# Kernel tuning notes

Measured on AMD Instinct MI355X. Metric: run time of the kernel, lower is better.

The kernel has to match this reference:

```python
import jax, jax.numpy as jnp
import numpy as np

HIDDEN = 512

def setup_inputs() -> dict:
    key = jax.random.key(0)
    kx, kq, kk, kv = jax.random.split(key, 4)
    B, S, H = 4, 4096, HIDDEN
    scale = 1.0 / np.sqrt(H)
    x = jax.random.normal(kx, (B, S, H), dtype=jnp.float32)
    # nn.Linear weights are [out, in]; y = x @ W.T
    Wq = jax.random.normal(kq, (H, H), dtype=jnp.float32) * scale
    Wk = jax.random.normal(kk, (H, H), dtype=jnp.float32) * scale
    Wv = jax.random.normal(kv, (H, H), dtype=jnp.float32) * scale
    return {"x": x, "Wq": Wq, "Wk": Wk, "Wv": Wv}

def reference(x, Wq, Wk, Wv):
    H = x.shape[-1]
    q = jnp.einsum('bsh,oh->bso', x, Wq)
    k = jnp.einsum('bsh,oh->bso', x, Wk)
    v = jnp.einsum('bsh,oh->bso', x, Wv)
    scores = jnp.einsum('bqh,bkh->bqk', q, k) / jnp.sqrt(jnp.asarray(H, x.dtype))
    att = jax.nn.softmax(scores, axis=-1)  # max-subtracted softmax, same math as manual version
    return jnp.einsum('bqk,bkh->bqh', att, v)
```

## Files before the change

### kernel.cpp

```cpp
#include <hip/hip_runtime.h>
#include <stdint.h>

typedef unsigned short u16;
typedef __bf16  bf16x8   __attribute__((ext_vector_type(8)));
typedef float   floatx4  __attribute__((ext_vector_type(4)));
typedef unsigned short ushortx4 __attribute__((ext_vector_type(4)));

__device__ __forceinline__ u16 f2bf(float f) {
  unsigned u = __builtin_bit_cast(unsigned, f);
  u += 0x7FFFu + ((u >> 16) & 1u);
  return (u16)(u >> 16);
}

#define GLD_LDS16(g, l)                                                        \
  __builtin_amdgcn_global_load_lds(                                            \
      (const __attribute__((address_space(1))) void*)(g),                      \
      (__attribute__((address_space(3))) void*)(l), 16, 0, 0)

#define VMW(N) asm volatile("s_waitcnt vmcnt(" #N ")" ::: "memory")

__global__ __launch_bounds__(256) void cvt_w(
    const float* __restrict__ Wq, const float* __restrict__ Wk,
    const float* __restrict__ Wv, u16* __restrict__ dst)
{
  const int z = blockIdx.y;
  const float* src = (z == 0) ? Wq : (z == 1) ? Wk : Wv;
  u16* d = dst + (size_t)z * 262144;
  const int idx = (blockIdx.x * 256 + threadIdx.x) * 8;
  const float4 lo = *(const float4*)&src[idx];
  const float4 hi = *(const float4*)&src[idx + 4];
  union { u16 h[8]; uint4 v; } pk;
  pk.h[0] = f2bf(lo.x); pk.h[1] = f2bf(lo.y); pk.h[2] = f2bf(lo.z); pk.h[3] = f2bf(lo.w);
  pk.h[4] = f2bf(hi.x); pk.h[5] = f2bf(hi.y); pk.h[6] = f2bf(hi.z); pk.h[7] = f2bf(hi.w);
  *(uint4*)&d[idx] = pk.v;
}

__global__ __launch_bounds__(256) void cvt_x(
    const float* __restrict__ X, u16* __restrict__ dst)
{
  const int idx = (blockIdx.x * 256 + threadIdx.x) * 8;
  const float4 lo = *(const float4*)&X[idx];
  const float4 hi = *(const float4*)&X[idx + 4];
  union { u16 h[8]; uint4 v; } pk;
  pk.h[0] = f2bf(lo.x); pk.h[1] = f2bf(lo.y); pk.h[2] = f2bf(lo.z); pk.h[3] = f2bf(lo.w);
  pk.h[4] = f2bf(hi.x); pk.h[5] = f2bf(hi.y); pk.h[6] = f2bf(hi.z); pk.h[7] = f2bf(hi.w);
  *(uint4*)&dst[idx] = pk.v;
}

__global__ __launch_bounds__(512, 2) void qkv8(
    const u16* __restrict__ X16, const u16* __restrict__ Wb,
    u16* __restrict__ qo, u16* __restrict__ ko, u16* __restrict__ vto)
{
  __shared__ u16 lds[65536];

  const int tid = threadIdx.x;
  const int w  = tid >> 6, l = tid & 63;
  const int lr = l & 15, lq = l >> 4;
  const int wA = (w & 1) * 16;
  const int wB = (w >> 1) * 16;

  const int bx = blockIdx.x;
  const int li = (bx & 7) * 48 + (bx >> 3);
  const int z  = li >> 7, u = li & 127;

  const u16* Ag; const u16* Bg; u16* dst; float sc; size_t ostr; int mb, nb;
  if (z < 2) {
    Ag = Wb + (size_t)z * 262144; Bg = X16;
    dst = z ? ko : qo; sc = z ? 1.0f : 0.06375871732f; ostr = 512;
    mb = (u & 1) * 256;  nb = (u >> 1) * 256;
  } else {
    Ag = X16; Bg = Wb + (size_t)2 * 262144;
    dst = vto; sc = 1.0f; ostr = 16384;
    mb = (u >> 1) * 256; nb = (u & 1) * 256;
  }

  floatx4 acc[8][4];
  const floatx4 fz = {0.f, 0.f, 0.f, 0.f};
#pragma unroll
  for (int i = 0; i < 8; ++i)
#pragma unroll
    for (int j = 0; j < 4; ++j) acc[i][j] = fz;

  auto stage = [&](int s) {
    const int ts = s >> 2, kind = s & 3;
    const int mat = kind & 1, h = kind >> 1;
    const u16* src = mat ? Bg : Ag;
    const int rbase = mat ? nb : mb;
    u16* dstl = &lds[(ts & 1) * 32768 + mat * 16384];
#pragma unroll
    for (int i = 0; i < 2; ++i) {
      const int c = i * 512 + tid;
      const int r = h * 128 + (c >> 3), k16 = c & 7;
      const int k16s = k16 ^ (r & 7);
      GLD_LDS16(src + (size_t)(rbase + r) * 512 + ts * 64 + k16s * 8,
                &dstl[r * 64 + k16 * 8]);
    }
  };

#pragma unroll
  for (int s = 0; s < 6; ++s) stage(s);
  VMW(4);
  __builtin_amdgcn_s_barrier();
  __builtin_amdgcn_sched_barrier(0);

  bf16x8 af[4][2];
  bf16x8 bf0[2][2], bf1[2][2];

#pragma unroll
  for (int t = 0; t < 8; ++t) {
#pragma unroll
    for (int qd = 0; qd < 4; ++qd) {
      const int fmh = qd >> 1;
      const int fnh = fmh ^ (qd & 1);
      const u16* AB = &lds[(t & 1) * 32768];
      const u16* BB = AB + 16384;

      if (qd == 0 || qd == 2) {
#pragma unroll
        for (int im = 0; im < 4; ++im) {
          const int rA = (fmh * 4 + im) * 32 + wA + lr;
#pragma unroll
          for (int ks = 0; ks < 2; ++ks) {
            const int k16p = (ks * 4 + lq) ^ (rA & 7);
            af[im][ks] = *(const bf16x8*)&AB[rA * 64 + k16p * 8];
          }
        }
      }
      if (qd == 0) {
#pragma unroll
        for (int jn = 0; jn < 2; ++jn) {
          const int rB = jn * 64 + wB + lr;
#pragma unroll
          for (int ks = 0; ks < 2; ++ks) {
            const int k16p = (ks * 4 + lq) ^ (rB & 7);
            bf0[jn][ks] = *(const bf16x8*)&BB[rB * 64 + k16p * 8];
          }
        }
      }
      if (qd == 1) {
#pragma unroll
        for (int jn = 0; jn < 2; ++jn) {
          const int rB = (2 + jn) * 64 + wB + lr;
#pragma unroll
          for (int ks = 0; ks < 2; ++ks) {
            const int k16p = (ks * 4 + lq) ^ (rB & 7);
            bf1[jn][ks] = *(const bf16x8*)&BB[rB * 64 + k16p * 8];
          }
        }
      }

      const int s = t * 4 + qd + 6;
      if (s < 32) stage(s);

      __builtin_amdgcn_sched_barrier(0);
      __builtin_amdgcn_s_barrier();
      asm volatile("s_waitcnt lgkmcnt(0)" ::: "memory");
      __builtin_amdgcn_sched_barrier(0);

      __builtin_amdgcn_s_setprio(1);
      if (fnh) {
#pragma unroll
        for (int im = 0; im < 4; ++im)
#pragma unroll
          for (int jn = 0; jn < 2; ++jn)
#pragma unroll
            for (int ks = 0; ks < 2; ++ks)
              acc[fmh * 4 + im][2 + jn] =
                  __builtin_amdgcn_mfma_f32_16x16x32_bf16(
                      af[im][ks], bf1[jn][ks], acc[fmh * 4 + im][2 + jn], 0, 0, 0);
      } else {
#pragma unroll
        for (int im = 0; im < 4; ++im)
#pragma unroll
          for (int jn = 0; jn < 2; ++jn)
#pragma unroll
            for (int ks = 0; ks < 2; ++ks)
              acc[fmh * 4 + im][jn] =
                  __builtin_amdgcn_mfma_f32_16x16x32_bf16(
                      af[im][ks], bf0[jn][ks], acc[fmh * 4 + im][jn], 0, 0, 0);
      }
      __builtin_amdgcn_s_setprio(0);

      if (qd == 3) {
        if (t < 6)        VMW(4);
        else if (t == 6)  VMW(0);
      }
      __builtin_amdgcn_s_barrier();
      __builtin_amdgcn_sched_barrier(0);
    }
  }

  const int cr = lq * 4;
#pragma unroll
  for (int fm = 0; fm < 8; ++fm)
#pragma unroll
    for (int fn = 0; fn < 4; ++fn) {
      const int mv = mb + fm * 32 + wA + cr;
      const int nv = nb + fn * 64 + wB + lr;
      ushortx4 pk;
#pragma unroll
      for (int r = 0; r < 4; ++r) pk[r] = f2bf(acc[fm][fn][r] * sc);
      *(ushortx4*)&dst[(size_t)nv * ostr + mv] = pk;
    }
}

__global__ __launch_bounds__(512, 2) void qk_exp8(
    const u16* __restrict__ q, const u16* __restrict__ k,
    u16* __restrict__ S, float* __restrict__ lsum)
{
  __shared__ u16 lds[65536];

  const int tid = threadIdx.x;
  const int w  = tid >> 6, l = tid & 63;
  const int lr = l & 15, lq = l >> 4;
  const int wA = (w & 1) * 16;
  const int wB = (w >> 1) * 16;
  const int kb0 = blockIdx.x * 256;
  const int qb0 = blockIdx.y * 256;
  const int b   = blockIdx.z;
  const size_t rb = (size_t)b * 4096;
  const u16* kg = k + rb * 512;
  const u16* qg = q + rb * 512;

  floatx4 acc[8][4];
  const floatx4 fz = {0.f, 0.f, 0.f, 0.f};
#pragma unroll
  for (int i = 0; i < 8; ++i)
#pragma unroll
    for (int j = 0; j < 4; ++j) acc[i][j] = fz;

  auto stage = [&](int s) {
    const int ts = s >> 2, kind = s & 3;
    const int mat = kind & 1, h = kind >> 1;
    const u16* src = mat ? qg : kg;
    const int rbase = mat ? qb0 : kb0;
    u16* dst = &lds[(ts & 1) * 32768 + mat * 16384];
#pragma unroll
    for (int i = 0; i < 2; ++i) {
      const int c = i * 512 + tid;
      const int r = h * 128 + (c >> 3), k16 = c & 7;
      const int k16s = k16 ^ (r & 7);
      GLD_LDS16(src + (size_t)(rbase + r) * 512 + ts * 64 + k16s * 8,
                &dst[r * 64 + k16 * 8]);
    }
  };

#pragma unroll
  for (int s = 0; s < 6; ++s) stage(s);
  VMW(4);
  __builtin_amdgcn_s_barrier();
  __builtin_amdgcn_sched_barrier(0);

  bf16x8 af[4][2];
  bf16x8 bf0[2][2], bf1[2][2];

#pragma unroll
  for (int t = 0; t < 8; ++t) {
#pragma unroll
    for (int qd = 0; qd < 4; ++qd) {
      const int fmh = qd >> 1;
      const int fnh = fmh ^ (qd & 1);
      const u16* AB = &lds[(t & 1) * 32768];
      const u16* BB = AB + 16384;

      if (qd == 0 || qd == 2) {
#pragma unroll
        for (int im = 0; im < 4; ++im) {
          const int rA = (fmh * 4 + im) * 32 + wA + lr;
#pragma unroll
          for (int ks = 0; ks < 2; ++ks) {
            const int k16p = (ks * 4 + lq) ^ (rA & 7);
            af[im][ks] = *(const bf16x8*)&AB[rA * 64 + k16p * 8];
          }
        }
      }
      if (qd == 0) {
#pragma unroll
        for (int jn = 0; jn < 2; ++jn) {
          const int rB = jn * 64 + wB + lr;
#pragma unroll
          for (int ks = 0; ks < 2; ++ks) {
            const int k16p = (ks * 4 + lq) ^ (rB & 7);
            bf0[jn][ks] = *(const bf16x8*)&BB[rB * 64 + k16p * 8];
          }
        }
      }
      if (qd == 1) {
#pragma unroll
        for (int jn = 0; jn < 2; ++jn) {
          const int rB = (2 + jn) * 64 + wB + lr;
#pragma unroll
          for (int ks = 0; ks < 2; ++ks) {
            const int k16p = (ks * 4 + lq) ^ (rB & 7);
            bf1[jn][ks] = *(const bf16x8*)&BB[rB * 64 + k16p * 8];
          }
        }
      }

      const int s = t * 4 + qd + 6;
      if (s < 32) stage(s);

      __builtin_amdgcn_sched_barrier(0);
      __builtin_amdgcn_s_barrier();
      asm volatile("s_waitcnt lgkmcnt(0)" ::: "memory");
      __builtin_amdgcn_sched_barrier(0);

      __builtin_amdgcn_s_setprio(1);
      if (fnh) {
#pragma unroll
        for (int im = 0; im < 4; ++im)
#pragma unroll
          for (int jn = 0; jn < 2; ++jn)
#pragma unroll
            for (int ks = 0; ks < 2; ++ks)
              acc[fmh * 4 + im][2 + jn] =
                  __builtin_amdgcn_mfma_f32_16x16x32_bf16(
                      af[im][ks], bf1[jn][ks], acc[fmh * 4 + im][2 + jn], 0, 0, 0);
      } else {
#pragma unroll
        for (int im = 0; im < 4; ++im)
#pragma unroll
          for (int jn = 0; jn < 2; ++jn)
#pragma unroll
            for (int ks = 0; ks < 2; ++ks)
              acc[fmh * 4 + im][jn] =
                  __builtin_amdgcn_mfma_f32_16x16x32_bf16(
                      af[im][ks], bf0[jn][ks], acc[fmh * 4 + im][jn], 0, 0, 0);
      }
      __builtin_amdgcn_s_setprio(0);

      if (qd == 3) {
        if (t < 6)        VMW(4);
        else if (t == 6)  VMW(0);
      }
      __builtin_amdgcn_s_barrier();
      __builtin_amdgcn_sched_barrier(0);
    }
  }

  const int cr = lq * 4;
  u16* Sb = S + ((size_t)b << 24);
  float js[4] = {0.f, 0.f, 0.f, 0.f};
#pragma unroll
  for (int fm = 0; fm < 8; ++fm)
#pragma unroll
    for (int fn = 0; fn < 4; ++fn) {
      const int key = kb0 + fm * 32 + wA + cr;
      const int qr  = qb0 + fn * 64 + wB + lr;
      ushortx4 pk;
      float s4 = 0.f;
#pragma unroll
      for (int r = 0; r < 4; ++r) {
        const float p = __builtin_amdgcn_exp2f(acc[fm][fn][r] - 17.31234049f);
        s4 += p;
        pk[r] = f2bf(p);
      }
      js[fn] += s4;
      *(ushortx4*)&Sb[(size_t)qr * 4096 + key] = pk;
    }
#pragma unroll
  for (int fn = 0; fn < 4; ++fn) {
    float s = js[fn];
    s += __shfl_xor(s, 16);
    s += __shfl_xor(s, 32);
    if (lq == 0)
      atomicAdd(&lsum[rb + qb0 + fn * 64 + wB + lr], s);
  }
}

#define PV_STG_A(TT, CK) do {                                                  \
    u16* dA_ = &lds[((TT) & 1) * 24576];                                       \
    _Pragma("unroll")                                                          \
    for (int i_ = 0; i_ < 2; ++i_) {                                           \
      const int c_ = i_ * 512 + tid, r_ = c_ >> 3, k_ = c_ & 7;                \
      GLD_LDS16(Sb + (size_t)(lm0 + (CK) * 128 + r_) * 4096 + (TT) * 64 +      \
                    (k_ ^ (r_ & 7)) * 8,                                       \
                &dA_[((CK) * 128 + r_) * 64 + k_ * 8]);                        \
    }                                                                          \
  } while (0)

#define PV_STG_B(TT) do {                                                      \
    u16* dB_ = &lds[((TT) & 1) * 24576 + 16384];                               \
    _Pragma("unroll")                                                          \
    for (int i_ = 0; i_ < 2; ++i_) {                                           \
      const int c_ = i_ * 512 + tid, r_ = c_ >> 3, k_ = c_ & 7;                \
      GLD_LDS16(vt + (size_t)(n0 + r_) * 16384 + bofs + (TT) * 64 +            \
                    (k_ ^ (r_ & 7)) * 8,                                       \
                &dB_[r_ * 64 + k_ * 8]);                                       \
    }                                                                          \
  } while (0)

#define PV_PH(T, PH, STAGE_CODE, TAIL_CODE) do {                               \
    const u16* AB_ = &lds[((T) & 1) * 24576];                                  \
    const u16* BB_ = AB_ + 16384;                                              \
    _Pragma("unroll")                                                          \
    for (int im_ = 0; im_ < 4; ++im_) {                                        \
      const int rA_ = ((PH) * 4 + im_) * 32 + wm16 + lr;                       \
      _Pragma("unroll")                                                        \
      for (int ks_ = 0; ks_ < 2; ++ks_) {                                      \
        const int kp_ = (ks_ * 4 + lq) ^ (rA_ & 7);                            \
        af[im_][ks_] = *(const bf16x8*)&AB_[rA_ * 64 + kp_ * 8];               \
      }                                                                        \
    }                                                                          \
    if ((PH) == 0) {                                                           \
      _Pragma("unroll")                                                        \
      for (int jn_ = 0; jn_ < 2; ++jn_) {                                      \
        const int rB_ = wn32 + jn_ * 16 + lr;                                  \
        _Pragma("unroll")                                                      \
        for (int ks_ = 0; ks_ < 2; ++ks_) {                                    \
          const int kp_ = (ks_ * 4 + lq) ^ (rB_ & 7);                          \
          bfv[jn_][ks_] = *(const bf16x8*)&BB_[rB_ * 64 + kp_ * 8];            \
        }                                                                      \
      }                                                                        \
    }                                                                          \
    STAGE_CODE;                                                                \
    __builtin_amdgcn_sched_barrier(0);                                         \
    __builtin_amdgcn_s_barrier();                                              \
    asm volatile("s_waitcnt lgkmcnt(0)" ::: "memory");                         \
    __builtin_amdgcn_sched_barrier(0);                                         \
    __builtin_amdgcn_s_setprio(1);                                             \
    _Pragma("unroll")                                                          \
    for (int im_ = 0; im_ < 4; ++im_)                                          \
      _Pragma("unroll")                                                        \
      for (int jn_ = 0; jn_ < 2; ++jn_)                                        \
        _Pragma("unroll")                                                      \
        for (int ks_ = 0; ks_ < 2; ++ks_)                                      \
          acc[(PH) * 4 + im_][jn_] = __builtin_amdgcn_mfma_f32_16x16x32_bf16(  \
              af[im_][ks_], bfv[jn_][ks_], acc[(PH) * 4 + im_][jn_], 0, 0, 0); \
    __builtin_amdgcn_s_setprio(0);                                             \
    TAIL_CODE;                                                                 \
    __builtin_amdgcn_s_barrier();                                              \
    __builtin_amdgcn_sched_barrier(0);                                         \
  } while (0)

#define PV_TILE(T, G_A1, G_A0B, VMCODE) do {                                   \
    PV_PH(T, 0, { if (G_A1) PV_STG_A((T) + 1, 1); }, (void)0);                 \
    PV_PH(T, 1, { if (G_A0B) { PV_STG_A((T) + 2, 0); PV_STG_B((T) + 2); } },   \
          VMCODE);                                                             \
  } while (0)

__global__ __launch_bounds__(512, 2) void pv8(
    const u16* __restrict__ S, const u16* __restrict__ vt,
    const float* __restrict__ lsum, float* __restrict__ out)
{
  __shared__ u16 lds[49152];

  const int tid = threadIdx.x;
  const int w  = tid >> 6, l = tid & 63;
  const int lr = l & 15, lq = l >> 4;
  const int wm16 = (w & 1) * 16;
  const int wn32 = (w >> 1) * 32;

  const int wg = blockIdx.x;
  const int li = (wg & 7) * 32 + (wg >> 3);
  const int n0 = (li & 3) * 128;
  const int m0 = (li >> 2) * 256;
  const int b  = m0 >> 12;
  const int lm0 = m0 & 4095;
  const u16* Sb = S + ((size_t)b << 24);
  const size_t bofs = (size_t)b * 4096;

  floatx4 acc[8][2];
  const floatx4 fz = {0.f, 0.f, 0.f, 0.f};
#pragma unroll
  for (int i = 0; i < 8; ++i) { acc[i][0] = fz; acc[i][1] = fz; }

  bf16x8 af[4][2], bfv[2][2];

  PV_STG_A(0, 0); PV_STG_B(0); PV_STG_A(0, 1); PV_STG_A(1, 0); PV_STG_B(1);
  VMW(4);
  __builtin_amdgcn_s_barrier();
  __builtin_amdgcn_sched_barrier(0);

  for (int t = 0; t < 62; t += 2) {
    PV_TILE(t,     1, 1, VMW(4));
    PV_TILE(t + 1, 1, 1, VMW(4));
  }
  PV_TILE(62, 1, 0, VMW(0));
  PV_TILE(63, 0, 0, (void)0);

  const int cr = lq * 4;
#pragma unroll
  for (int fm = 0; fm < 8; ++fm) {
    const int m = m0 + fm * 32 + wm16 + cr;
    float inv[4];
#pragma unroll
    for (int r = 0; r < 4; ++r) inv[r] = 1.0f / lsum[m + r];
#pragma unroll
    for (int jn = 0; jn < 2; ++jn) {
      const int n = n0 + wn32 + jn * 16 + lr;
#pragma unroll
      for (int r = 0; r < 4; ++r)
        out[(size_t)(m + r) * 512 + n] = acc[fm][jn][r] * inv[r];
    }
  }
}

extern "C" void kernel_launch(void* const* d_in, const int* in_sizes, int n_in,
                              void* d_out, int out_size, void* d_ws, size_t ws_size,
                              hipStream_t stream) {
  (void)in_sizes; (void)n_in; (void)out_size; (void)ws_size;
  const float* x  = (const float*)d_in[0];
  const float* Wq = (const float*)d_in[1];
  const float* Wk = (const float*)d_in[2];
  const float* Wv = (const float*)d_in[3];
  float* out = (float*)d_out;
  u16* ws  = (u16*)d_ws;
  u16* qw  = ws;
  u16* kw  = qw + (size_t)16384 * 512;
  u16* vw  = kw + (size_t)16384 * 512;
  u16* x16 = vw + (size_t)16384 * 512;
  u16* wb  = x16 + (size_t)16384 * 512;
  u16* Sp  = wb + (size_t)3 * 262144;
  float* lsum = (float*)(Sp + ((size_t)4 << 24));

  hipMemsetAsync(lsum, 0, 16384 * sizeof(float), stream);
  cvt_w<<<dim3(128, 3), dim3(256), 0, stream>>>(Wq, Wk, Wv, wb);
  cvt_x<<<dim3(4096), dim3(256), 0, stream>>>(x, x16);
  qkv8<<<dim3(384), dim3(512), 0, stream>>>(x16, wb, qw, kw, vw);
  qk_exp8<<<dim3(16, 16, 4), dim3(512), 0, stream>>>(qw, kw, Sp, lsum);
  pv8<<<dim3(256), dim3(512), 0, stream>>>(Sp, vw, lsum, out);
}
```

Before: 279.6 us.

## Software-pipeline LDS fragment reads one quarter ahead in QK kernel

The qk_exp8 main loop now loads the A/B fragments for the next MFMA quarter after the current quarter's MFMAs, instead of loading them before the MFMAs. It also prefetches the first fragments of the next double-buffer stage. This drops the per-quarter barrier plus the lgkmcnt(0) wait that used to sit before the MFMAs, so LDS read latency can overlap with matrix math. In exchange, the vmcnt waits get finer-grained, fragment registers stay live across iterations, and correctness now depends on careful barrier placement relative to the global-to-LDS staging.

```diff
diff --git a/kernel.cpp b/kernel.cpp
--- a/kernel.cpp
+++ b/kernel.cpp
@@ -204,6 +204,34 @@
     }
 }
 
+#define QK_READ_A(BUFP, HALF)                                                  \
+  do {                                                                         \
+    const u16* AB_ = &lds[(BUFP) * 32768];                                     \
+    _Pragma("unroll")                                                          \
+    for (int im_ = 0; im_ < 4; ++im_) {                                        \
+      const int rA_ = ((HALF) * 4 + im_) * 32 + wA + lr;                       \
+      _Pragma("unroll")                                                        \
+      for (int ks_ = 0; ks_ < 2; ++ks_) {                                      \
+        const int kp_ = (ks_ * 4 + lq) ^ (rA_ & 7);                            \
+        af[im_][ks_] = *(const bf16x8*)&AB_[rA_ * 64 + kp_ * 8];               \
+      }                                                                        \
+    }                                                                          \
+  } while (0)
+
+#define QK_READ_B(BUFP, HALF, DST)                                             \
+  do {                                                                         \
+    const u16* BB_ = &lds[(BUFP) * 32768 + 16384];                             \
+    _Pragma("unroll")                                                          \
+    for (int jn_ = 0; jn_ < 2; ++jn_) {                                        \
+      const int rB_ = ((HALF) * 2 + jn_) * 64 + wB + lr;                       \
+      _Pragma("unroll")                                                        \
+      for (int ks_ = 0; ks_ < 2; ++ks_) {                                      \
+        const int kp_ = (ks_ * 4 + lq) ^ (rB_ & 7);                            \
+        DST[jn_][ks_] = *(const bf16x8*)&BB_[rB_ * 64 + kp_ * 8];              \
+      }                                                                        \
+    }                                                                          \
+  } while (0)
+
 __global__ __launch_bounds__(512, 2) void qk_exp8(
     const u16* __restrict__ q, const u16* __restrict__ k,
     u16* __restrict__ S, float* __restrict__ lsum)
@@ -245,14 +273,16 @@
     }
   };
 
+  bf16x8 af[4][2];
+  bf16x8 bf0[2][2], bf1[2][2];
+
 #pragma unroll
   for (int s = 0; s < 6; ++s) stage(s);
   VMW(4);
   __builtin_amdgcn_s_barrier();
   __builtin_amdgcn_sched_barrier(0);
-
-  bf16x8 af[4][2];
-  bf16x8 bf0[2][2], bf1[2][2];
+  QK_READ_A(0, 0);
+  QK_READ_B(0, 0, bf0);
 
 #pragma unroll
   for (int t = 0; t < 8; ++t) {
@@ -260,50 +290,6 @@
     for (int qd = 0; qd < 4; ++qd) {
       const int fmh = qd >> 1;
       const int fnh = fmh ^ (qd & 1);
-      const u16* AB = &lds[(t & 1) * 32768];
-      const u16* BB = AB + 16384;
-
-      if (qd == 0 || qd == 2) {
-#pragma unroll
-        for (int im = 0; im < 4; ++im) {
-          const int rA = (fmh * 4 + im) * 32 + wA + lr;
-#pragma unroll
-          for (int ks = 0; ks < 2; ++ks) {
-            const int k16p = (ks * 4 + lq) ^ (rA & 7);
-            af[im][ks] = *(const bf16x8*)&AB[rA * 64 + k16p * 8];
-          }
-        }
-      }
-      if (qd == 0) {
-#pragma unroll
-        for (int jn = 0; jn < 2; ++jn) {
-          const int rB = jn * 64 + wB + lr;
-#pragma unroll
-          for (int ks = 0; ks < 2; ++ks) {
-            const int k16p = (ks * 4 + lq) ^ (rB & 7);
-            bf0[jn][ks] = *(const bf16x8*)&BB[rB * 64 + k16p * 8];
-          }
-        }
-      }
-      if (qd == 1) {
-#pragma unroll
-        for (int jn = 0; jn < 2; ++jn) {
-          const int rB = (2 + jn) * 64 + wB + lr;
-#pragma unroll
-          for (int ks = 0; ks < 2; ++ks) {
-            const int k16p = (ks * 4 + lq) ^ (rB & 7);
-            bf1[jn][ks] = *(const bf16x8*)&BB[rB * 64 + k16p * 8];
-          }
-        }
-      }
-
-      const int s = t * 4 + qd + 6;
-      if (s < 32) stage(s);
-
-      __builtin_amdgcn_sched_barrier(0);
-      __builtin_amdgcn_s_barrier();
-      asm volatile("s_waitcnt lgkmcnt(0)" ::: "memory");
-      __builtin_amdgcn_sched_barrier(0);
 
       __builtin_amdgcn_s_setprio(1);
       if (fnh) {
@@ -328,12 +314,23 @@
                       af[im][ks], bf0[jn][ks], acc[fmh * 4 + im][jn], 0, 0, 0);
       }
       __builtin_amdgcn_s_setprio(0);
-
-      if (qd == 3) {
-        if (t < 6)        VMW(4);
-        else if (t == 6)  VMW(0);
-      }
-      __builtin_amdgcn_s_barrier();
+      __builtin_amdgcn_sched_barrier(0);
+
+      if (qd == 0) QK_READ_B(t & 1, 1, bf1);
+      if (qd == 1) QK_READ_A(t & 1, 1);
+      if (qd == 3 && t < 7) {
+        QK_READ_A((t + 1) & 1, 0);
+        QK_READ_B((t + 1) & 1, 0, bf0);
+      }
+
+      const int s = t * 4 + qd + 6;
+      if (s < 32) stage(s);
+
+      if (qd == 2) { if (t < 6) VMW(6); else if (t == 6) VMW(4); }
+      if (qd == 3) { if (t < 6) VMW(4); else if (t == 6) VMW(0); }
+
+      __builtin_amdgcn_sched_barrier(0);
+      if (t < 7 || qd < 3) __builtin_amdgcn_s_barrier();
       __builtin_amdgcn_sched_barrier(0);
     }
   }
```

New measurement: 300.0 us (median of 2 runs). 7.3% more time.
